# Optimization experiments

Measured on AMD Instinct MI355X. Metric: run time of the kernel, lower is better.

The kernel has to match this reference:

```python
import jax, jax.numpy as jnp
import numpy as np

NT, NC = 100000, 25000
ETT, ECT = 800000, 400000
DIN_T, DIN_C = 64, 32
H, C = 4, 32
HID = H * C  # 128
SLOPE = 0.2  # GATConv LeakyReLU negative slope


def setup_inputs() -> dict:
    key = jax.random.key(0)
    ks = jax.random.split(key, 24)
    def p(i, shape, s=0.05):
        return jax.random.normal(ks[i], shape, dtype=jnp.float32) * s
    return {
        'x_target': jax.random.normal(ks[0], (NT, DIN_T), dtype=jnp.float32),
        'x_context': jax.random.normal(ks[1], (NC, DIN_C), dtype=jnp.float32),
        'edge_tt': jax.random.randint(ks[2], (2, ETT), 0, NT),
        'edge_ct_src': jax.random.randint(ks[3], (ECT,), 0, NC),
        'edge_ct_dst': jax.random.randint(ks[4], (ECT,), 0, NT),
        'W_pre_t': p(5, (DIN_T, HID)), 'b_pre_t': jnp.zeros((HID,), jnp.float32),
        'W_pre_c': p(6, (DIN_C, HID)), 'b_pre_c': jnp.zeros((HID,), jnp.float32),
        'W_sd': p(7, (HID, HID)), 'att_src_sd': p(8, (H, C)), 'att_dst_sd': p(9, (H, C)), 'b_sd': jnp.zeros((HID,), jnp.float32),
        'W_ds': p(10, (HID, HID)), 'att_src_ds': p(11, (H, C)), 'att_dst_ds': p(12, (H, C)), 'b_ds': jnp.zeros((HID,), jnp.float32),
        'W_ct_src': p(13, (HID, HID)), 'W_ct_dst': p(14, (HID, HID)), 'att_src_ct': p(15, (H, C)), 'att_dst_ct': p(16, (H, C)), 'b_ct': jnp.zeros((HID,), jnp.float32),
        'W_out': p(17, (HID, HID)), 'b_out': jnp.zeros((HID,), jnp.float32),
    }


def _gat(h_src, h_dst, att_s, att_d, src, dst, n_dst, bias):
    # h_src: [N_src,H,C] transformed src feats; h_dst: [N_dst,H,C]
    a_s = jnp.einsum('nhc,hc->nh', h_src, att_s)  # [N_src,H]
    a_d = jnp.einsum('nhc,hc->nh', h_dst, att_d)  # [N_dst,H]
    e = a_s[src] + a_d[dst]                        # [E,H]
    e = jnp.where(e > 0, e, SLOPE * e)             # LeakyReLU(0.2)
    m = jax.ops.segment_max(e, dst, num_segments=n_dst)  # stable softmax per dst
    ex = jnp.exp(e - m[dst])
    den = jax.ops.segment_sum(ex, dst, num_segments=n_dst)
    alpha = ex / den[dst]                          # [E,H]
    msg = h_src[src] * alpha[:, :, None]           # [E,H,C]
    out = jax.ops.segment_sum(msg, dst, num_segments=n_dst)
    return out.reshape(n_dst, H * C) + bias


def reference(x_target, x_context, edge_tt, edge_ct_src, edge_ct_dst,
              W_pre_t, b_pre_t, W_pre_c, b_pre_c,
              W_sd, att_src_sd, att_dst_sd, b_sd,
              W_ds, att_src_ds, att_dst_ds, b_ds,
              W_ct_src, W_ct_dst, att_src_ct, att_dst_ct, b_ct,
              W_out, b_out):
    # HeteroDictLinear pretransform + relu
    h_t = jax.nn.relu(x_target @ W_pre_t + b_pre_t)   # [NT,128]
    h_c = jax.nn.relu(x_context @ W_pre_c + b_pre_c)  # [NC,128]
    res = h_t
    # DirGATConv on (target,to,target): forward + reversed, each w/ self-loops
    loops = jnp.arange(NT)
    src_f = jnp.concatenate([edge_tt[0], loops]); dst_f = jnp.concatenate([edge_tt[1], loops])
    src_r = jnp.concatenate([edge_tt[1], loops]); dst_r = jnp.concatenate([edge_tt[0], loops])
    hs = (h_t @ W_sd).reshape(NT, H, C)
    out_sd = _gat(hs, hs, att_src_sd, att_dst_sd, src_f, dst_f, NT, b_sd)
    hd = (h_t @ W_ds).reshape(NT, H, C)
    out_ds = _gat(hd, hd, att_src_ds, att_dst_ds, src_r, dst_r, NT, b_ds)
    out_tt = 0.5 * out_sd + 0.5 * out_ds  # (1-alpha), alpha with alpha=0.5
    # bipartite GATConv on (context,to,target), no self loops
    hcs = (h_c @ W_ct_src).reshape(NC, H, C)
    htd = (h_t @ W_ct_dst).reshape(NT, H, C)
    out_ct = _gat(hcs, htd, att_src_ct, att_dst_ct, edge_ct_src, edge_ct_dst, NT, b_ct)
    # HeteroConv aggr='mean' over the two edge types hitting 'target'
    x = 0.5 * (out_tt + out_ct)
    x = jax.nn.relu(x + res)  # skip connection + relu
    return x @ W_out + b_out
```

## Files before the change

kernel.cpp:

```cpp
#include <hip/hip_runtime.h>
#include <cstdint>
#include <cstddef>

typedef unsigned short u16;
typedef unsigned int u32;

#define NT 100000
#define NC 25000
#define ETT 800000
#define ECT 400000
#define SLOPE 0.2f
#define LOG2E 1.4426950408889634f
#define OFFS (NT + 4)

#define NBK 782
#define NBLK 256
#define CHT ((ETT + NBLK - 1) / NBLK)
#define CHC ((ECT + NBLK - 1) / NBLK)
#define TOTC (3 * NBK * NBLK)
#define NSB ((TOTC + 4095) / 4096)
#define FILL_CAP 4096

#define PT_BLK ((NT + 63) / 64)
#define CT_BLK ((NC + 63) / 64)

#define LROWS1 782
#define LROWS2 781
#define GOH 50048
#define G1BLK (GOH / 16)
#define G2BLK ((NT - GOH + 15) / 16)
#define OB1 (GOH / 64)
#define OB2 ((NT - GOH + 63) / 64)

typedef __attribute__((ext_vector_type(8))) short bf16x8;
typedef __attribute__((ext_vector_type(4))) float f32x4;

__device__ __forceinline__ u16 f2bf(float f) {
  u32 u = __float_as_uint(f);
  u32 r = (u >> 16) & 1u;
  return (u16)((u + 0x7fffu + r) >> 16);
}
__device__ __forceinline__ float lof(u32 p) { return __uint_as_float(p << 16); }
__device__ __forceinline__ float hif(u32 p) { return __uint_as_float(p & 0xffff0000u); }

__device__ __forceinline__ void compute_bpre(const int* __restrict__ bsum, int* s_bpre) {
  const int t = threadIdx.x;
  const int v = (t < NSB) ? bsum[t] : 0;
  s_bpre[t] = v;
  __syncthreads();
  for (int d = 1; d < 256; d <<= 1) {
    const int u = (t >= d) ? s_bpre[t - d] : 0;
    __syncthreads();
    s_bpre[t] += u;
    __syncthreads();
  }
  const int incl = s_bpre[t];
  __syncthreads();
  s_bpre[t] = incl - v;
  __syncthreads();
}

__global__ __launch_bounds__(256) void transform_hist_kernel(
    const int* __restrict__ tt_src, const int* __restrict__ tt_dst,
    const int* __restrict__ ect_d, int* __restrict__ cntblk,
    const float* __restrict__ Wsd, const float* __restrict__ AsSd, const float* __restrict__ AdSd,
    const float* __restrict__ Wds, const float* __restrict__ AsDs, const float* __restrict__ AdDs,
    const float* __restrict__ Wout,
    u16* __restrict__ bf_sd, u16* __restrict__ bf_ds, u16* __restrict__ bf_out,
    const float* __restrict__ Wcd, const float* __restrict__ attD,
    const float* __restrict__ bsd, const float* __restrict__ bds, const float* __restrict__ bct,
    float* __restrict__ cbias,
    const float* __restrict__ x_t, const float* __restrict__ Wpt, const float* __restrict__ bpt,
    u16* __restrict__ h_t, float* __restrict__ aD,
    const float* __restrict__ x_c, const float* __restrict__ Wpc, const float* __restrict__ bpc,
    const float* __restrict__ Wcs, const float* __restrict__ attS,
    u16* __restrict__ hc_bf, float* __restrict__ aS_c)
{
  __shared__ __align__(16) char smem[51200];
  const int t = threadIdx.x;

  if (blockIdx.x < NBLK) {
    int* h = (int*)smem;
    const int b = blockIdx.x;
    for (int i = t; i < 3 * NBK; i += 256) h[i] = 0;
    __syncthreads();
    const int lo = b * CHT, hi = min(lo + CHT, ETT);
    for (int i = lo + t; i < hi; i += 256) {
      atomicAdd(&h[tt_dst[i] >> 7], 1);
      atomicAdd(&h[NBK + (tt_src[i] >> 7)], 1);
    }
    const int lo2 = b * CHC, hi2 = min(lo2 + CHC, ECT);
    for (int i = lo2 + t; i < hi2; i += 256)
      atomicAdd(&h[2 * NBK + (ect_d[i] >> 7)], 1);
    __syncthreads();
    for (int i = t; i < 3 * NBK; i += 256)
      cntblk[(size_t)i * NBLK + b] = h[i];
    return;
  }

  const int b = blockIdx.x - NBLK;

  if (b < 4) {
    if (b == 3) {
      if (t < 128) cbias[t] = 0.25f * bsd[t] + 0.25f * bds[t] + 0.5f * bct[t];
      return;
    }
    float* fS = (float*)smem;
    float* fD = fS + 512;
    const float* W = (b == 0) ? Wsd : (b == 1) ? Wds : Wout;
    const float* As = (b == 0) ? AsSd : AsDs;
    const float* Ad = (b == 0) ? AdSd : AdDs;
    u16* out = (b == 0) ? bf_sd : (b == 1) ? bf_ds : bf_out;
    const int tiles = (b == 2) ? 8 : 9;
    if (b < 2) {
      if (t < 128) {
        for (int hh = 0; hh < 4; ++hh) {
          float s1 = 0.f, s2 = 0.f;
          for (int c = 0; c < 32; ++c) {
            const float wv = W[t * 128 + hh * 32 + c];
            s1 = fmaf(wv, As[hh * 32 + c], s1);
            s2 = fmaf(wv, Ad[hh * 32 + c], s2);
          }
          fS[t * 4 + hh] = s1 * LOG2E; fD[t * 4 + hh] = s2 * LOG2E;
        }
      }
      __syncthreads();
    }
    const int total = tiles * 4 * 64 * 8;
    for (int i = t; i < total; i += 256) {
      const int j = i & 7, lane = (i >> 3) & 63, ks = (i >> 9) & 3, ti = i >> 11;
      const int k = ks * 32 + (lane >> 4) * 8 + j;
      const int n = ti * 16 + (lane & 15);
      float v;
      if (n < 128) v = W[k * 128 + n];
      else if (n < 132) v = fS[k * 4 + (n - 128)];
      else if (n < 136) v = fD[k * 4 + (n - 132)];
      else v = 0.f;
      out[i] = f2bf(v);
    }
    return;
  }

  if (b < 4 + PT_BLK) {
    float (*s_xt)[68] = (float(*)[68])smem;
    float (*s_W)[128] = (float(*)[128])(smem + 17408);
    float* s_fold     = (float*)(smem + 17408 + 16384);
    const int row0 = (b - 4) * 64;
    for (int g = 0; g < 4; ++g) {
      const int lr = g * 16 + (t >> 4);
      const int k4 = (t & 15) * 4;
      const int grow = row0 + lr;
      float4 f = make_float4(0.f, 0.f, 0.f, 0.f);
      if (grow < NT) f = *(const float4*)(x_t + (size_t)grow * 64 + k4);
      s_xt[k4 + 0][lr] = f.x; s_xt[k4 + 1][lr] = f.y;
      s_xt[k4 + 2][lr] = f.z; s_xt[k4 + 3][lr] = f.w;
    }
    if (t < 128) {
      for (int hh = 0; hh < 4; ++hh) {
        float s = 0.f;
        for (int c = 0; c < 32; ++c)
          s = fmaf(Wcd[t * 128 + hh * 32 + c], attD[hh * 32 + c], s);
        s_fold[t * 4 + hh] = s * LOG2E;
      }
    }
    const int rg = t >> 4;
    const int cg = t & 15;
    float acc[4][8];
    for (int r = 0; r < 4; ++r)
      for (int j = 0; j < 8; ++j)
        acc[r][j] = bpt[cg * 4 + (j & 3) + (j >> 2) * 64];
    for (int kc = 0; kc < 64; kc += 32) {
      for (int j = 0; j < 4; ++j) {
        const int idx = t + j * 256;
        const int k = idx >> 5, c4 = (idx & 31) * 4;
        *(float4*)&s_W[k][c4] = *(const float4*)(Wpt + (size_t)(kc + k) * 128 + c4);
      }
      __syncthreads();
#pragma unroll 8
      for (int k = 0; k < 32; ++k) {
        const float4 xa = *(const float4*)&s_xt[kc + k][rg * 4];
        const float4 w0 = *(const float4*)&s_W[k][cg * 4];
        const float4 w1 = *(const float4*)&s_W[k][cg * 4 + 64];
        const float xr[4] = {xa.x, xa.y, xa.z, xa.w};
        for (int r = 0; r < 4; ++r) {
          acc[r][0] = fmaf(xr[r], w0.x, acc[r][0]);
          acc[r][1] = fmaf(xr[r], w0.y, acc[r][1]);
          acc[r][2] = fmaf(xr[r], w0.z, acc[r][2]);
          acc[r][3] = fmaf(xr[r], w0.w, acc[r][3]);
          acc[r][4] = fmaf(xr[r], w1.x, acc[r][4]);
          acc[r][5] = fmaf(xr[r], w1.y, acc[r][5]);
          acc[r][6] = fmaf(xr[r], w1.z, acc[r][6]);
          acc[r][7] = fmaf(xr[r], w1.w, acc[r][7]);
        }
      }
      __syncthreads();
    }
    for (int r = 0; r < 4; ++r) {
      const int grow = row0 + rg * 4 + r;
      float v[8];
      for (int j = 0; j < 8; ++j) v[j] = fmaxf(acc[r][j], 0.f);
      float p0 = 0.f, p1 = 0.f, p2 = 0.f, p3 = 0.f;
      for (int j = 0; j < 8; ++j) {
        const int col = cg * 4 + (j & 3) + ((j >> 2) * 64);
        const float4 f4 = *(const float4*)&s_fold[col * 4];
        p0 = fmaf(v[j], f4.x, p0); p1 = fmaf(v[j], f4.y, p1);
        p2 = fmaf(v[j], f4.z, p2); p3 = fmaf(v[j], f4.w, p3);
      }
      if (grow < NT) {
        uint2 pk;
        pk.x = (u32)f2bf(v[0]) | ((u32)f2bf(v[1]) << 16);
        pk.y = (u32)f2bf(v[2]) | ((u32)f2bf(v[3]) << 16);
        *(uint2*)(h_t + (size_t)grow * 128 + cg * 4) = pk;
        pk.x = (u32)f2bf(v[4]) | ((u32)f2bf(v[5]) << 16);
        pk.y = (u32)f2bf(v[6]) | ((u32)f2bf(v[7]) << 16);
        *(uint2*)(h_t + (size_t)grow * 128 + cg * 4 + 64) = pk;
      }
      for (int m = 1; m < 16; m <<= 1) {
        p0 += __shfl_xor(p0, m); p1 += __shfl_xor(p1, m);
        p2 += __shfl_xor(p2, m); p3 += __shfl_xor(p3, m);
      }
      if (cg == 0 && grow < NT)
        *(float4*)(aD + (size_t)grow * 4) = make_float4(p0, p1, p2, p3);
    }
    return;
  }

  {
    float (*s_ht)[68]  = (float(*)[68])smem;
    float (*s_W2)[128] = (float(*)[128])(smem + 34816);
    float (*s_xc)[68]  = (float(*)[68])smem;
    const int row0 = (b - 4 - PT_BLK) * 64;
    for (int g = 0; g < 2; ++g) {
      const int lr = g * 32 + (t >> 3);
      const int k4 = (t & 7) * 4;
      const int grow = row0 + lr;
      float4 f = make_float4(0.f, 0.f, 0.f, 0.f);
      if (grow < NC) f = *(const float4*)(x_c + (size_t)grow * 32 + k4);
      s_xc[k4 + 0][lr] = f.x; s_xc[k4 + 1][lr] = f.y;
      s_xc[k4 + 2][lr] = f.z; s_xc[k4 + 3][lr] = f.w;
    }
    for (int j = 0; j < 4; ++j) {
      const int idx = t + j * 256;
      const int k = idx >> 5, c4 = (idx & 31) * 4;
      *(float4*)&s_W2[k][c4] = *(const float4*)(Wpc + (size_t)k * 128 + c4);
    }
    __syncthreads();
    const int rg = t >> 4, cg = t & 15;
    float acc1[4][8];
    for (int r = 0; r < 4; ++r)
      for (int j = 0; j < 8; ++j)
        acc1[r][j] = bpc[cg * 4 + (j & 3) + (j >> 2) * 64];
#pragma unroll 8
    for (int k = 0; k < 32; ++k) {
      const float4 xa = *(const float4*)&s_xc[k][rg * 4];
      const float4 w0 = *(const float4*)&s_W2[k][cg * 4];
      const float4 w1 = *(const float4*)&s_W2[k][cg * 4 + 64];
      const float xr[4] = {xa.x, xa.y, xa.z, xa.w};
      for (int r = 0; r < 4; ++r) {
        acc1[r][0] = fmaf(xr[r], w0.x, acc1[r][0]);
        acc1[r][1] = fmaf(xr[r], w0.y, acc1[r][1]);
        acc1[r][2] = fmaf(xr[r], w0.z, acc1[r][2]);
        acc1[r][3] = fmaf(xr[r], w0.w, acc1[r][3]);
        acc1[r][4] = fmaf(xr[r], w1.x, acc1[r][4]);
        acc1[r][5] = fmaf(xr[r], w1.y, acc1[r][5]);
        acc1[r][6] = fmaf(xr[r], w1.z, acc1[r][6]);
        acc1[r][7] = fmaf(xr[r], w1.w, acc1[r][7]);
      }
    }
    __syncthreads();
    for (int r = 0; r < 4; ++r) {
      const int lr = rg * 4 + r;
      for (int j = 0; j < 8; ++j) {
        const int col = cg * 4 + (j & 3) + ((j >> 2) * 64);
        s_ht[col][lr] = fmaxf(acc1[r][j], 0.f);
      }
    }
    for (int j = 0; j < 4; ++j) {
      const int idx = t + j * 256;
      const int k = idx >> 5, c4 = (idx & 31) * 4;
      *(float4*)&s_W2[k][c4] = *(const float4*)(Wcs + (size_t)k * 128 + c4);
    }
    __syncthreads();
    float acc2[4][8];
    for (int r = 0; r < 4; ++r)
      for (int j = 0; j < 8; ++j) acc2[r][j] = 0.f;
    for (int kc = 0; kc < 128; kc += 32) {
#pragma unroll 8
      for (int k = 0; k < 32; ++k) {
        const float4 xa = *(const float4*)&s_ht[kc + k][rg * 4];
        const float4 w0 = *(const float4*)&s_W2[k][cg * 4];
        const float4 w1 = *(const float4*)&s_W2[k][cg * 4 + 64];
        const float xr[4] = {xa.x, xa.y, xa.z, xa.w};
        for (int r = 0; r < 4; ++r) {
          acc2[r][0] = fmaf(xr[r], w0.x, acc2[r][0]);
          acc2[r][1] = fmaf(xr[r], w0.y, acc2[r][1]);
          acc2[r][2] = fmaf(xr[r], w0.z, acc2[r][2]);
          acc2[r][3] = fmaf(xr[r], w0.w, acc2[r][3]);
          acc2[r][4] = fmaf(xr[r], w1.x, acc2[r][4]);
          acc2[r][5] = fmaf(xr[r], w1.y, acc2[r][5]);
          acc2[r][6] = fmaf(xr[r], w1.z, acc2[r][6]);
          acc2[r][7] = fmaf(xr[r], w1.w, acc2[r][7]);
        }
      }
      if (kc < 96) {
        __syncthreads();
        for (int j = 0; j < 4; ++j) {
          const int idx = t + j * 256;
          const int k = idx >> 5, c4 = (idx & 31) * 4;
          *(float4*)&s_W2[k][c4] = *(const float4*)(Wcs + (size_t)(kc + 32 + k) * 128 + c4);
        }
        __syncthreads();
      }
    }
    const int h2 = cg >> 3;
    const float4 at0 = *(const float4*)(attS + cg * 4);
    const float4 at1 = *(const float4*)(attS + cg * 4 + 64);
    for (int r = 0; r < 4; ++r) {
      const int grow = row0 + rg * 4 + r;
      float pa = acc2[r][0] * at0.x + acc2[r][1] * at0.y +
                 acc2[r][2] * at0.z + acc2[r][3] * at0.w;
      float pb = acc2[r][4] * at1.x + acc2[r][5] * at1.y +
                 acc2[r][6] * at1.z + acc2[r][7] * at1.w;
      if (grow < NC) {
        uint2 pk;
        pk.x = (u32)f2bf(acc2[r][0]) | ((u32)f2bf(acc2[r][1]) << 16);
        pk.y = (u32)f2bf(acc2[r][2]) | ((u32)f2bf(acc2[r][3]) << 16);
        *(uint2*)(hc_bf + (size_t)grow * 128 + cg * 4) = pk;
        pk.x = (u32)f2bf(acc2[r][4]) | ((u32)f2bf(acc2[r][5]) << 16);
        pk.y = (u32)f2bf(acc2[r][6]) | ((u32)f2bf(acc2[r][7]) << 16);
        *(uint2*)(hc_bf + (size_t)grow * 128 + cg * 4 + 64) = pk;
      }
      for (int m = 1; m < 8; m <<= 1) {
        pa += __shfl_xor(pa, m);
        pb += __shfl_xor(pb, m);
      }
      if ((cg & 7) == 0 && grow < NC) {
        aS_c[(size_t)grow * 4 + h2] = pa * LOG2E;
        aS_c[(size_t)grow * 4 + 2 + h2] = pb * LOG2E;
      }
    }
  }
}

__global__ __launch_bounds__(256) void scan2_blk_kernel(const int* __restrict__ in,
    int* __restrict__ out, int* __restrict__ bsum)
{
  const int t = threadIdx.x, b = blockIdx.x;
  const int idx = b * 4096 + t * 16;
  int v[16];
  int s = 0;
  if (idx < TOTC) {
#pragma unroll
    for (int q = 0; q < 4; ++q) {
      const int4 qq = *(const int4*)(in + idx + q * 4);
      v[q * 4 + 0] = s; s += qq.x;
      v[q * 4 + 1] = s; s += qq.y;
      v[q * 4 + 2] = s; s += qq.z;
      v[q * 4 + 3] = s; s += qq.w;
    }
  } else {
    for (int j = 0; j < 16; ++j) v[j] = 0;
  }
  __shared__ int sh[256];
  sh[t] = s;
  __syncthreads();
  for (int d = 1; d < 256; d <<= 1) {
    const int u = (t >= d) ? sh[t - d] : 0;
    __syncthreads();
    sh[t] += u;
    __syncthreads();
  }
  const int excl = (t == 0) ? 0 : sh[t - 1];
  if (idx < TOTC) {
#pragma unroll
    for (int q = 0; q < 4; ++q) {
      int4 qo;
      qo.x = excl + v[q * 4 + 0]; qo.y = excl + v[q * 4 + 1];
      qo.z = excl + v[q * 4 + 2]; qo.w = excl + v[q * 4 + 3];
      *(int4*)(out + idx + q * 4) = qo;
    }
  }
  if (t == 255) bsum[b] = sh[255];
}

__device__ __forceinline__ void logits2_body(float (*lds)[16][148], int blk, int rbase,
    const short* __restrict__ A, const short* __restrict__ Bsd, const short* __restrict__ Bds,
    u16* __restrict__ hs, float* __restrict__ aSsd, float* __restrict__ aDsd,
    u16* __restrict__ hd, float* __restrict__ aSds, float* __restrict__ aDds, int M)
{
  const int t = threadIdx.x;
  const int wv = t >> 6, lane = t & 63;
  const int quad = lane >> 4, l16 = lane & 15;
  const int row0 = rbase + blk * 64 + wv * 16;
  const int arow = min(row0 + l16, M - 1);
  const short* ap = A + (size_t)arow * 128 + quad * 8;
  bf16x8 af[4];
  for (int ks = 0; ks < 4; ++ks) af[ks] = *(const bf16x8*)(ap + ks * 32);
  const int row = row0 + l16;
  const int idx = lane & 7, rr = lane >> 3;
  for (int pass = 0; pass < 2; ++pass) {
    const short* B = pass ? Bds : Bsd;
    u16* outb = pass ? hd : hs;
    float* aS = pass ? aSds : aSsd;
    float* aD = pass ? aDds : aDsd;
    f32x4 acc[9];
    for (int ti = 0; ti < 9; ++ti) acc[ti] = (f32x4){0.f, 0.f, 0.f, 0.f};
    for (int ks = 0; ks < 4; ++ks)
      for (int ti = 0; ti < 9; ++ti) {
        const bf16x8 bf = *(const bf16x8*)(B + ((ti * 4 + ks) * 64 + lane) * 8);
        acc[ti] = __builtin_amdgcn_mfma_f32_16x16x32_bf16(af[ks], bf, acc[ti], 0, 0, 0);
      }
    for (int ti = 0; ti < 9; ++ti)
      for (int r = 0; r < 4; ++r)
        lds[wv][quad * 4 + r][ti * 16 + l16] = acc[ti][r];
    __syncthreads();
    if (row < M) {
      for (int g = 0; g < 8; ++g) {
        const f32x4 v = *(const f32x4*)&lds[wv][l16][g * 16 + quad * 4];
        uint2 pk;
        pk.x = (u32)f2bf(v[0]) | ((u32)f2bf(v[1]) << 16);
        pk.y = (u32)f2bf(v[2]) | ((u32)f2bf(v[3]) << 16);
        *(uint2*)(outb + (size_t)row * 128 + g * 16 + quad * 4) = pk;
      }
    }
    for (int p = 0; p < 2; ++p) {
      const int lr = p * 8 + rr;
      const int n = row0 + lr;
      if (n < M) {
        const float v = lds[wv][lr][128 + idx];
        if (idx < 4) aS[(size_t)n * 4 + idx] = v;
        else aD[(size_t)n * 4 + idx - 4] = v;
      }
    }
    __syncthreads();
  }
}

__global__ __launch_bounds__(256) void bin_logits2_kernel(
    const int* __restrict__ tt_src, const int* __restrict__ tt_dst,
    const int* __restrict__ ect_s, const int* __restrict__ ect_d,
    const int* __restrict__ scanned, const int* __restrict__ bsum, u32* __restrict__ bin,
    const short* __restrict__ A, const short* __restrict__ Bsd, const short* __restrict__ Bds,
    u16* __restrict__ hs, float* __restrict__ aSsd, float* __restrict__ aDsd,
    u16* __restrict__ hd, float* __restrict__ aSds, float* __restrict__ aDds, int M)
{
  __shared__ __align__(16) float ldsf[4][16][148];
  const int t = threadIdx.x;

  if (blockIdx.x < NBLK) {
    int* cur = (int*)&ldsf[0][0][0];
    int* s_bpre = cur + 3 * NBK;
    compute_bpre(bsum, s_bpre);
    const int b = blockIdx.x;
    for (int i = t; i < 3 * NBK; i += 256) {
      const int idx = i * NBLK + b;
      cur[i] = scanned[idx] + s_bpre[idx >> 12];
    }
    __syncthreads();
    const int lo = b * CHT, hi = min(lo + CHT, ETT);
    for (int i = lo + t; i < hi; i += 256) {
      const int s = tt_src[i], d = tt_dst[i];
      int p = atomicAdd(&cur[d >> 7], 1);
      bin[p] = ((u32)(d & 127) << 17) | (u32)s;
      p = atomicAdd(&cur[NBK + (s >> 7)], 1);
      bin[p] = ((u32)(s & 127) << 17) | (u32)d;
    }
    const int lo2 = b * CHC, hi2 = min(lo2 + CHC, ECT);
    for (int i = lo2 + t; i < hi2; i += 256) {
      const int s = ect_s[i], d = ect_d[i];
      const int p = atomicAdd(&cur[2 * NBK + (d >> 7)], 1);
      bin[p] = ((u32)(d & 127) << 17) | (u32)s;
    }
    return;
  }
  logits2_body(ldsf, blockIdx.x - NBLK, 0, A, Bsd, Bds,
               hs, aSsd, aDsd, hd, aSds, aDds, M);
}

__global__ __launch_bounds__(256) void fill_logits2_kernel(
    const int* __restrict__ scanned, const int* __restrict__ bsum, const u32* __restrict__ bin,
    int* __restrict__ offs, int* __restrict__ big_el,
    const short* __restrict__ A, const short* __restrict__ Bsd, const short* __restrict__ Bds,
    u16* __restrict__ hs, float* __restrict__ aSsd, float* __restrict__ aDsd,
    u16* __restrict__ hd, float* __restrict__ aSds, float* __restrict__ aDds, int M)
{
  __shared__ __align__(16) float ldsf[4][16][148];
  const int t = threadIdx.x;

  if (blockIdx.x < 3 * NBK) {
    int* base0 = (int*)&ldsf[0][0][0];
    int* s_cnt = base0;
    int* s_exc = base0 + 128;
    int* s_cur = base0 + 256;
    int* s_bpre = base0 + 384;
    int* s_el = base0 + 640;
    compute_bpre(bsum, s_bpre);
    const int rel = blockIdx.x / NBK;
    const int bucket = blockIdx.x - rel * NBK;
    if (t < 128) s_cnt[t] = 0;
    const int bi = blockIdx.x * NBLK;
    const int base = scanned[bi] + s_bpre[bi >> 12];
    const int nxt = (blockIdx.x == 3 * NBK - 1)
                        ? (2 * ETT + ECT)
                        : scanned[bi + NBLK] + s_bpre[(bi + NBLK) >> 12];
    __syncthreads();
    const int size = nxt - base;
    for (int i = t; i < size; i += 256)
      atomicAdd(&s_cnt[bin[base + i] >> 17], 1);
    __syncthreads();
    if (t < 128) s_exc[t] = s_cnt[t];
    __syncthreads();
    for (int d = 1; d < 128; d <<= 1) {
      int v = 0;
      if (t < 128 && t >= d) v = s_exc[t - d];
      __syncthreads();
      if (t < 128) s_exc[t] += v;
      __syncthreads();
    }
    const int relbase = rel * ETT;
    const int obase = base - relbase;
    int* off_rel = offs + (size_t)rel * OFFS;
    const int node0 = bucket * 128;
    if (t < 128) {
      const int excl = s_exc[t] - s_cnt[t];
      s_cur[t] = excl;
      if (node0 + t < NT) off_rel[node0 + t] = obase + excl;
    }
    if (t == 0 && bucket == NBK - 1) off_rel[NT] = obase + size;
    __syncthreads();
    int* el_rel = big_el + relbase;
    if (size <= FILL_CAP) {
      for (int i = t; i < size; i += 256) {
        const u32 e = bin[base + i];
        const int pos = atomicAdd(&s_cur[e >> 17], 1);
        s_el[pos] = (int)(e & 0x1FFFFu);
      }
      __syncthreads();
      for (int i = t; i < size; i += 256)
        el_rel[obase + i] = s_el[i];
    } else {
      for (int i = t; i < size; i += 256) {
        const u32 e = bin[base + i];
        const int pos = atomicAdd(&s_cur[e >> 17], 1);
        el_rel[obase + pos] = (int)(e & 0x1FFFFu);
      }
    }
    return;
  }
  logits2_body(ldsf, blockIdx.x - 3 * NBK, GOH, A, Bsd, Bds,
               hs, aSsd, aDsd, hd, aSds, aDds, M);
}

__device__ __forceinline__ void mfma_out_body(float (*lds)[16][132], int row0,
    const short* __restrict__ A, const short* __restrict__ B,
    const float* __restrict__ bias, float* __restrict__ out, int M)
{
  const int t = threadIdx.x;
  const int wv = t >> 6, lane = t & 63;
  const int quad = lane >> 4, l16 = lane & 15;
  const int r0 = row0 + wv * 16;
  const int arow = min(r0 + l16, M - 1);
  const short* ap = A + (size_t)arow * 128 + quad * 8;
  bf16x8 af[4];
  for (int ks = 0; ks < 4; ++ks) af[ks] = *(const bf16x8*)(ap + ks * 32);
  f32x4 acc[8];
  for (int ti = 0; ti < 8; ++ti) acc[ti] = (f32x4){0.f, 0.f, 0.f, 0.f};
  for (int ks = 0; ks < 4; ++ks)
    for (int ti = 0; ti < 8; ++ti) {
      const bf16x8 bf = *(const bf16x8*)(B + ((ti * 4 + ks) * 64 + lane) * 8);
      acc[ti] = __builtin_amdgcn_mfma_f32_16x16x32_bf16(af[ks], bf, acc[ti], 0, 0, 0);
    }
  for (int ti = 0; ti < 8; ++ti)
    for (int r = 0; r < 4; ++r)
      lds[wv][quad * 4 + r][ti * 16 + l16] = acc[ti][r];
  __syncthreads();
  const int row = r0 + l16;
  if (row < M) {
    for (int g = 0; g < 8; ++g) {
      const int col = g * 16 + quad * 4;
      f32x4 v = *(const f32x4*)&lds[wv][l16][col];
      const f32x4 b4 = *(const f32x4*)(bias + col);
      v = v + b4;
      *(f32x4*)(out + (size_t)row * 128 + col) = v;
    }
  }
}

__global__ __launch_bounds__(256) void mfma_out_kernel(
    const short* __restrict__ A, const short* __restrict__ B,
    const float* __restrict__ bias, float* __restrict__ out, int rbase, int M)
{
  __shared__ __align__(16) float lds[4][16][132];
  mfma_out_body(lds, rbase + blockIdx.x * 64, A, B, bias, out, M);
}

__device__ __forceinline__ void gat_pipe16(const int* __restrict__ off,
    const int* __restrict__ el, const float* __restrict__ aS, const float* __restrict__ aD,
    const u16* __restrict__ hb, int d, int h, int cb, int self_loop, float w,
    float* __restrict__ acc)
{
  const float ad = aD[(size_t)d * 4 + h];
  const int beg = off[d];
  const int m = off[d + 1] - beg;
  const int cnt = m + self_loop;
  if (cnt <= 0) return;
  float den = 0.f;
  float a0 = 0.f, a1 = 0.f, a2 = 0.f, a3 = 0.f, a4 = 0.f, a5 = 0.f, a6 = 0.f, a7 = 0.f;
  int sB = (1 < m) ? el[beg + 1] : d;
  {
    const int sA0 = (0 < m) ? el[beg] : d;
    float eA = aS[(size_t)sA0 * 4 + h];
    uint4 pA = *(const uint4*)(hb + (size_t)sA0 * 128 + cb);
    for (int k = 0; k < cnt; ++k) {
      const int sC = (k + 2 < m) ? el[beg + k + 2] : d;
      const float eB = aS[(size_t)sB * 4 + h];
      const uint4 pB = *(const uint4*)(hb + (size_t)sB * 128 + cb);
      float ea = eA + ad;
      ea = ea > 0.f ? ea : SLOPE * ea;
      const float ex = exp2f(ea);
      den += ex;
      a0 = fmaf(ex, lof(pA.x), a0); a1 = fmaf(ex, hif(pA.x), a1);
      a2 = fmaf(ex, lof(pA.y), a2); a3 = fmaf(ex, hif(pA.y), a3);
      a4 = fmaf(ex, lof(pA.z), a4); a5 = fmaf(ex, hif(pA.z), a5);
      a6 = fmaf(ex, lof(pA.w), a6); a7 = fmaf(ex, hif(pA.w), a7);
      eA = eB; pA = pB; sB = sC;
    }
  }
  const float s = w / den;
  acc[0] = fmaf(a0, s, acc[0]); acc[1] = fmaf(a1, s, acc[1]);
  acc[2] = fmaf(a2, s, acc[2]); acc[3] = fmaf(a3, s, acc[3]);
  acc[4] = fmaf(a4, s, acc[4]); acc[5] = fmaf(a5, s, acc[5]);
  acc[6] = fmaf(a6, s, acc[6]); acc[7] = fmaf(a7, s, acc[7]);
}

__device__ __forceinline__ void gather_body(int d,
    const int* __restrict__ off_f, const int* __restrict__ el_f,
    const float* __restrict__ aS_sd, const float* __restrict__ aD_sd, const u16* __restrict__ hs,
    const int* __restrict__ off_r, const int* __restrict__ el_r,
    const float* __restrict__ aS_ds, const float* __restrict__ aD_ds, const u16* __restrict__ hd,
    const int* __restrict__ off_c, const int* __restrict__ el_c,
    const float* __restrict__ aS_ct, const float* __restrict__ aD_ct, const u16* __restrict__ hc,
    const u16* __restrict__ skip, const float* __restrict__ cbias, u16* __restrict__ x)
{
  const int lg = threadIdx.x & 15;
  const int h = lg >> 2;
  const int cb = lg * 8;
  float acc[8];
  for (int i = 0; i < 8; ++i) acc[i] = 0.f;
  gat_pipe16(off_f, el_f, aS_sd, aD_sd, hs, d, h, cb, 1, 0.25f, acc);
  gat_pipe16(off_r, el_r, aS_ds, aD_ds, hd, d, h, cb, 1, 0.25f, acc);
  gat_pipe16(off_c, el_c, aS_ct, aD_ct, hc, d, h, cb, 0, 0.5f, acc);
  const uint4 sk = *(const uint4*)(skip + (size_t)d * 128 + cb);
  const float4 cb0 = *(const float4*)(cbias + cb);
  const float4 cb1 = *(const float4*)(cbias + cb + 4);
  const float o0 = fmaxf(acc[0] + cb0.x + lof(sk.x), 0.f);
  const float o1 = fmaxf(acc[1] + cb0.y + hif(sk.x), 0.f);
  const float o2 = fmaxf(acc[2] + cb0.z + lof(sk.y), 0.f);
  const float o3 = fmaxf(acc[3] + cb0.w + hif(sk.y), 0.f);
  const float o4 = fmaxf(acc[4] + cb1.x + lof(sk.z), 0.f);
  const float o5 = fmaxf(acc[5] + cb1.y + hif(sk.z), 0.f);
  const float o6 = fmaxf(acc[6] + cb1.z + lof(sk.w), 0.f);
  const float o7 = fmaxf(acc[7] + cb1.w + hif(sk.w), 0.f);
  uint4 r;
  r.x = (u32)f2bf(o0) | ((u32)f2bf(o1) << 16);
  r.y = (u32)f2bf(o2) | ((u32)f2bf(o3) << 16);
  r.z = (u32)f2bf(o4) | ((u32)f2bf(o5) << 16);
  r.w = (u32)f2bf(o6) | ((u32)f2bf(o7) << 16);
  *(uint4*)(x + (size_t)d * 128 + cb) = r;
}

__global__ __launch_bounds__(256) void gather_all_kernel(
    const int* __restrict__ off_f, const int* __restrict__ el_f,
    const float* __restrict__ aS_sd, const float* __restrict__ aD_sd, const u16* __restrict__ hs,
    const int* __restrict__ off_r, const int* __restrict__ el_r,
    const float* __restrict__ aS_ds, const float* __restrict__ aD_ds, const u16* __restrict__ hd,
    const int* __restrict__ off_c, const int* __restrict__ el_c,
    const float* __restrict__ aS_ct, const float* __restrict__ aD_ct, const u16* __restrict__ hc,
    const u16* __restrict__ skip, const float* __restrict__ cbias, u16* __restrict__ x)
{
  const int d = blockIdx.x * 16 + (threadIdx.x >> 4);
  if (d >= NT) return;
  gather_body(d, off_f, el_f, aS_sd, aD_sd, hs, off_r, el_r, aS_ds, aD_ds, hd,
              off_c, el_c, aS_ct, aD_ct, hc, skip, cbias, x);
}

__global__ __launch_bounds__(256) void gather_out_kernel(
    const int* __restrict__ off_f, const int* __restrict__ el_f,
    const float* __restrict__ aS_sd, const float* __restrict__ aD_sd, const u16* __restrict__ hs,
    const int* __restrict__ off_r, const int* __restrict__ el_r,
    const float* __restrict__ aS_ds, const float* __restrict__ aD_ds, const u16* __restrict__ hd,
    const int* __restrict__ off_c, const int* __restrict__ el_c,
    const float* __restrict__ aS_ct, const float* __restrict__ aD_ct, const u16* __restrict__ hc,
    const u16* __restrict__ skip, const float* __restrict__ cbias, u16* __restrict__ x,
    const short* __restrict__ B, const float* __restrict__ bias, float* __restrict__ out, int M)
{
  __shared__ __align__(16) float lds[4][16][132];
  if (blockIdx.x < G2BLK) {
    const int d = GOH + blockIdx.x * 16 + (threadIdx.x >> 4);
    if (d >= NT) return;
    gather_body(d, off_f, el_f, aS_sd, aD_sd, hs, off_r, el_r, aS_ds, aD_ds, hd,
                off_c, el_c, aS_ct, aD_ct, hc, skip, cbias, x);
    return;
  }
  mfma_out_body(lds, (blockIdx.x - G2BLK) * 64, (const short*)x, B, bias, out, M);
}

extern "C" void kernel_launch(void* const* d_in, const int* in_sizes, int n_in,
                              void* d_out, int out_size, void* d_ws, size_t ws_size,
                              hipStream_t stream)
{
  const float* x_t   = (const float*)d_in[0];
  const float* x_c   = (const float*)d_in[1];
  const int*   e_tt  = (const int*)d_in[2];
  const int*   ect_s = (const int*)d_in[3];
  const int*   ect_d = (const int*)d_in[4];
  const float* Wpt = (const float*)d_in[5];   const float* bpt = (const float*)d_in[6];
  const float* Wpc = (const float*)d_in[7];   const float* bpc = (const float*)d_in[8];
  const float* Wsd = (const float*)d_in[9];   const float* As_sd = (const float*)d_in[10];
  const float* Ad_sd = (const float*)d_in[11]; const float* bsd = (const float*)d_in[12];
  const float* Wds = (const float*)d_in[13];  const float* As_ds = (const float*)d_in[14];
  const float* Ad_ds = (const float*)d_in[15]; const float* bds = (const float*)d_in[16];
  const float* Wcs = (const float*)d_in[17];  const float* Wcd = (const float*)d_in[18];
  const float* As_ct = (const float*)d_in[19]; const float* Ad_ct = (const float*)d_in[20];
  const float* bct = (const float*)d_in[21];
  const float* Wout = (const float*)d_in[22]; const float* bout = (const float*)d_in[23];

  char* p = (char*)d_ws;
  size_t off = 0;
  auto alloc = [&](size_t bytes) { char* r = p + off; off += (bytes + 255) & ~(size_t)255; return r; };
  u16* ht_bf   = (u16*)alloc((size_t)NT * 128 * 2);
  u16* hs_bf   = (u16*)alloc((size_t)NT * 128 * 2);
  u16* hd_bf   = (u16*)alloc((size_t)NT * 128 * 2);
  u16* hc_bf   = (u16*)alloc((size_t)NC * 128 * 2);
  u16* x_bf    = (u16*)alloc((size_t)NT * 128 * 2);
  float* aS_sd = (float*)alloc((size_t)NT * 4 * 4);
  float* aD_sd = (float*)alloc((size_t)NT * 4 * 4);
  float* aS_ds = (float*)alloc((size_t)NT * 4 * 4);
  float* aD_ds = (float*)alloc((size_t)NT * 4 * 4);
  float* aS_ct = (float*)alloc((size_t)NC * 4 * 4);
  float* aD_ct = (float*)alloc((size_t)NT * 4 * 4);
  int* cntblk  = (int*)alloc((size_t)TOTC * 4);
  int* scanned = (int*)alloc((size_t)TOTC * 4);
  u32* bin     = (u32*)alloc((size_t)(2 * ETT + ECT) * 4);
  int* big_el  = (int*)alloc((size_t)(2 * ETT + ECT) * 4);
  int* offs    = (int*)alloc((size_t)3 * OFFS * 4);
  int* bsum    = (int*)alloc((size_t)NSB * 4);
  float* cbias   = (float*)alloc(128 * 4);
  u16* bfrag_sd  = (u16*)alloc((size_t)9 * 4 * 64 * 8 * 2);
  u16* bfrag_ds  = (u16*)alloc((size_t)9 * 4 * 64 * 8 * 2);
  u16* bfrag_out = (u16*)alloc((size_t)8 * 4 * 64 * 8 * 2);

  int* off_f = offs;
  int* off_r = offs + OFFS;
  int* off_c = offs + 2 * OFFS;
  int* el_f = big_el;
  int* el_r = big_el + ETT;
  int* el_c = big_el + 2 * ETT;

  const int* tt_src = e_tt;
  const int* tt_dst = e_tt + ETT;

  transform_hist_kernel<<<NBLK + 4 + PT_BLK + CT_BLK, 256, 0, stream>>>(
      tt_src, tt_dst, ect_d, cntblk,
      Wsd, As_sd, Ad_sd, Wds, As_ds, Ad_ds, Wout,
      bfrag_sd, bfrag_ds, bfrag_out,
      Wcd, Ad_ct, bsd, bds, bct, cbias,
      x_t, Wpt, bpt, ht_bf, aD_ct,
      x_c, Wpc, bpc, Wcs, As_ct, hc_bf, aS_ct);

  scan2_blk_kernel<<<NSB, 256, 0, stream>>>(cntblk, scanned, bsum);

  bin_logits2_kernel<<<NBLK + LROWS1, 256, 0, stream>>>(
      tt_src, tt_dst, ect_s, ect_d, scanned, bsum, bin,
      (const short*)ht_bf, (const short*)bfrag_sd, (const short*)bfrag_ds,
      hs_bf, aS_sd, aD_sd, hd_bf, aS_ds, aD_ds, NT);

  fill_logits2_kernel<<<3 * NBK + LROWS2, 256, 0, stream>>>(
      scanned, bsum, bin, offs, big_el,
      (const short*)ht_bf, (const short*)bfrag_sd, (const short*)bfrag_ds,
      hs_bf, aS_sd, aD_sd, hd_bf, aS_ds, aD_ds, NT);

  gather_all_kernel<<<G1BLK, 256, 0, stream>>>(
      off_f, el_f, aS_sd, aD_sd, hs_bf,
      off_r, el_r, aS_ds, aD_ds, hd_bf,
      off_c, el_c, aS_ct, aD_ct, hc_bf,
      ht_bf, cbias, x_bf);

  gather_out_kernel<<<G2BLK + OB1, 256, 0, stream>>>(
      off_f, el_f, aS_sd, aD_sd, hs_bf,
      off_r, el_r, aS_ds, aD_ds, hd_bf,
      off_c, el_c, aS_ct, aD_ct, hc_bf,
      ht_bf, cbias, x_bf,
      (const short*)bfrag_out, bout, (float*)d_out, NT);

  mfma_out_kernel<<<OB2, 256, 0, stream>>>((const short*)x_bf, (const short*)bfrag_out,
                                           bout, (float*)d_out, GOH, NT);
}
```

Before: 409.7 us.

## Move all logits GEMM into bin kernel, slim fill kernel, direct-store output GEMM

```diff
diff --git a/kernel.cpp b/kernel.cpp
--- a/kernel.cpp
+++ b/kernel.cpp
@@ -23,12 +23,11 @@
 
 #define PT_BLK ((NT + 63) / 64)
 #define CT_BLK ((NC + 63) / 64)
-
-#define LROWS1 782
-#define LROWS2 781
+#define GM_BLK ((NT + 63) / 64)
+
 #define GOH 50048
 #define G1BLK (GOH / 16)
-#define G2BLK ((NT - GOH + 15) / 16)
+#define G2BLK ((NT - GOH) / 16)
 #define OB1 (GOH / 64)
 #define OB2 ((NT - GOH + 63) / 64)
 
@@ -383,7 +382,7 @@
   if (t == 255) bsum[b] = sh[255];
 }
 
-__device__ __forceinline__ void logits2_body(float (*lds)[16][148], int blk, int rbase,
+__device__ __forceinline__ void logits2_body(float (*lds)[16][148], int blk,
     const short* __restrict__ A, const short* __restrict__ Bsd, const short* __restrict__ Bds,
     u16* __restrict__ hs, float* __restrict__ aSsd, float* __restrict__ aDsd,
     u16* __restrict__ hd, float* __restrict__ aSds, float* __restrict__ aDds, int M)
@@ -391,7 +390,7 @@
   const int t = threadIdx.x;
   const int wv = t >> 6, lane = t & 63;
   const int quad = lane >> 4, l16 = lane & 15;
-  const int row0 = rbase + blk * 64 + wv * 16;
+  const int row0 = blk * 64 + wv * 16;
   const int arow = min(row0 + l16, M - 1);
   const short* ap = A + (size_t)arow * 128 + quad * 8;
   bf16x8 af[4];
@@ -473,85 +472,71 @@
     }
     return;
   }
-  logits2_body(ldsf, blockIdx.x - NBLK, 0, A, Bsd, Bds,
+  logits2_body(ldsf, blockIdx.x - NBLK, A, Bsd, Bds,
                hs, aSsd, aDsd, hd, aSds, aDds, M);
 }
 
-__global__ __launch_bounds__(256) void fill_logits2_kernel(
-    const int* __restrict__ scanned, const int* __restrict__ bsum, const u32* __restrict__ bin,
-    int* __restrict__ offs, int* __restrict__ big_el,
-    const short* __restrict__ A, const short* __restrict__ Bsd, const short* __restrict__ Bds,
-    u16* __restrict__ hs, float* __restrict__ aSsd, float* __restrict__ aDsd,
-    u16* __restrict__ hd, float* __restrict__ aSds, float* __restrict__ aDds, int M)
-{
-  __shared__ __align__(16) float ldsf[4][16][148];
+__global__ __launch_bounds__(256) void bucket_fill_kernel(const int* __restrict__ scanned,
+    const int* __restrict__ bsum, const u32* __restrict__ bin,
+    int* __restrict__ offs, int* __restrict__ big_el)
+{
+  __shared__ int s_cnt[128], s_exc[128], s_cur[128], s_bpre[256];
+  __shared__ int s_el[FILL_CAP];
   const int t = threadIdx.x;
-
-  if (blockIdx.x < 3 * NBK) {
-    int* base0 = (int*)&ldsf[0][0][0];
-    int* s_cnt = base0;
-    int* s_exc = base0 + 128;
-    int* s_cur = base0 + 256;
-    int* s_bpre = base0 + 384;
-    int* s_el = base0 + 640;
-    compute_bpre(bsum, s_bpre);
-    const int rel = blockIdx.x / NBK;
-    const int bucket = blockIdx.x - rel * NBK;
-    if (t < 128) s_cnt[t] = 0;
-    const int bi = blockIdx.x * NBLK;
-    const int base = scanned[bi] + s_bpre[bi >> 12];
-    const int nxt = (blockIdx.x == 3 * NBK - 1)
-                        ? (2 * ETT + ECT)
-                        : scanned[bi + NBLK] + s_bpre[(bi + NBLK) >> 12];
-    __syncthreads();
-    const int size = nxt - base;
+  compute_bpre(bsum, s_bpre);
+  const int rel = blockIdx.x / NBK;
+  const int bucket = blockIdx.x - rel * NBK;
+  if (t < 128) s_cnt[t] = 0;
+  const int bi = blockIdx.x * NBLK;
+  const int base = scanned[bi] + s_bpre[bi >> 12];
+  const int nxt = (blockIdx.x == 3 * NBK - 1)
+                      ? (2 * ETT + ECT)
+                      : scanned[bi + NBLK] + s_bpre[(bi + NBLK) >> 12];
+  __syncthreads();
+  const int size = nxt - base;
+  for (int i = t; i < size; i += 256)
+    atomicAdd(&s_cnt[bin[base + i] >> 17], 1);
+  __syncthreads();
+  if (t < 128) s_exc[t] = s_cnt[t];
+  __syncthreads();
+  for (int d = 1; d < 128; d <<= 1) {
+    int v = 0;
+    if (t < 128 && t >= d) v = s_exc[t - d];
+    __syncthreads();
+    if (t < 128) s_exc[t] += v;
+    __syncthreads();
+  }
+  const int relbase = rel * ETT;
+  const int obase = base - relbase;
+  int* off_rel = offs + (size_t)rel * OFFS;
+  const int node0 = bucket * 128;
+  if (t < 128) {
+    const int excl = s_exc[t] - s_cnt[t];
+    s_cur[t] = excl;
+    if (node0 + t < NT) off_rel[node0 + t] = obase + excl;
+  }
+  if (t == 0 && bucket == NBK - 1) off_rel[NT] = obase + size;
+  __syncthreads();
+  int* el_rel = big_el + relbase;
+  if (size <= FILL_CAP) {
+    for (int i = t; i < size; i += 256) {
+      const u32 e = bin[base + i];
+      const int pos = atomicAdd(&s_cur[e >> 17], 1);
+      s_el[pos] = (int)(e & 0x1FFFFu);
+    }
+    __syncthreads();
     for (int i = t; i < size; i += 256)
-      atomicAdd(&s_cnt[bin[base + i] >> 17], 1);
-    __syncthreads();
-    if (t < 128) s_exc[t] = s_cnt[t];
-    __syncthreads();
-    for (int d = 1; d < 128; d <<= 1) {
-      int v = 0;
-      if (t < 128 && t >= d) v = s_exc[t - d];
-      __syncthreads();
-      if (t < 128) s_exc[t] += v;
-      __syncthreads();
-    }
-    const int relbase = rel * ETT;
-    const int obase = base - relbase;
-    int* off_rel = offs + (size_t)rel * OFFS;
-    const int node0 = bucket * 128;
-    if (t < 128) {
-      const int excl = s_exc[t] - s_cnt[t];
-      s_cur[t] = excl;
-      if (node0 + t < NT) off_rel[node0 + t] = obase + excl;
-    }
-    if (t == 0 && bucket == NBK - 1) off_rel[NT] = obase + size;
-    __syncthreads();
-    int* el_rel = big_el + relbase;
-    if (size <= FILL_CAP) {
-      for (int i = t; i < size; i += 256) {
-        const u32 e = bin[base + i];
-        const int pos = atomicAdd(&s_cur[e >> 17], 1);
-        s_el[pos] = (int)(e & 0x1FFFFu);
-      }
-      __syncthreads();
-      for (int i = t; i < size; i += 256)
-        el_rel[obase + i] = s_el[i];
-    } else {
-      for (int i = t; i < size; i += 256) {
-        const u32 e = bin[base + i];
-        const int pos = atomicAdd(&s_cur[e >> 17], 1);
-        el_rel[obase + pos] = (int)(e & 0x1FFFFu);
-      }
-    }
-    return;
-  }
-  logits2_body(ldsf, blockIdx.x - 3 * NBK, GOH, A, Bsd, Bds,
-               hs, aSsd, aDsd, hd, aSds, aDds, M);
-}
-
-__device__ __forceinline__ void mfma_out_body(float (*lds)[16][132], int row0,
+      el_rel[obase + i] = s_el[i];
+  } else {
+    for (int i = t; i < size; i += 256) {
+      const u32 e = bin[base + i];
+      const int pos = atomicAdd(&s_cur[e >> 17], 1);
+      el_rel[obase + pos] = (int)(e & 0x1FFFFu);
+    }
+  }
+}
+
+__device__ __forceinline__ void mfma_out_direct(int row0,
     const short* __restrict__ A, const short* __restrict__ B,
     const float* __restrict__ bias, float* __restrict__ out, int M)
 {
@@ -570,18 +555,17 @@
       const bf16x8 bf = *(const bf16x8*)(B + ((ti * 4 + ks) * 64 + lane) * 8);
       acc[ti] = __builtin_amdgcn_mfma_f32_16x16x32_bf16(af[ks], bf, acc[ti], 0, 0, 0);
     }
-  for (int ti = 0; ti < 8; ++ti)
-    for (int r = 0; r < 4; ++r)
-      lds[wv][quad * 4 + r][ti * 16 + l16] = acc[ti][r];
-  __syncthreads();
-  const int row = r0 + l16;
-  if (row < M) {
-    for (int g = 0; g < 8; ++g) {
-      const int col = g * 16 + quad * 4;
-      f32x4 v = *(const f32x4*)&lds[wv][l16][col];
-      const f32x4 b4 = *(const f32x4*)(bias + col);
-      v = v + b4;
-      *(f32x4*)(out + (size_t)row * 128 + col) = v;
+  float bcol[8];
+#pragma unroll
+  for (int ti = 0; ti < 8; ++ti) bcol[ti] = bias[ti * 16 + l16];
+#pragma unroll
+  for (int r = 0; r < 4; ++r) {
+    const int row = r0 + quad * 4 + r;
+    if (row < M) {
+      float* orow = out + (size_t)row * 128 + l16;
+#pragma unroll
+      for (int ti = 0; ti < 8; ++ti)
+        orow[ti * 16] = acc[ti][r] + bcol[ti];
     }
   }
 }
@@ -590,8 +574,7 @@
     const short* __restrict__ A, const short* __restrict__ B,
     const float* __restrict__ bias, float* __restrict__ out, int rbase, int M)
 {
-  __shared__ __align__(16) float lds[4][16][132];
-  mfma_out_body(lds, rbase + blockIdx.x * 64, A, B, bias, out, M);
+  mfma_out_direct(rbase + blockIdx.x * 64, A, B, bias, out, M);
 }
 
 __device__ __forceinline__ void gat_pipe16(const int* __restrict__ off,
@@ -694,7 +677,6 @@
     const u16* __restrict__ skip, const float* __restrict__ cbias, u16* __restrict__ x,
     const short* __restrict__ B, const float* __restrict__ bias, float* __restrict__ out, int M)
 {
-  __shared__ __align__(16) float lds[4][16][132];
   if (blockIdx.x < G2BLK) {
     const int d = GOH + blockIdx.x * 16 + (threadIdx.x >> 4);
     if (d >= NT) return;
@@ -702,7 +684,7 @@
                 off_c, el_c, aS_ct, aD_ct, hc, skip, cbias, x);
     return;
   }
-  mfma_out_body(lds, (blockIdx.x - G2BLK) * 64, (const short*)x, B, bias, out, M);
+  mfma_out_direct((blockIdx.x - G2BLK) * 64, (const short*)x, B, bias, out, M);
 }
 
 extern "C" void kernel_launch(void* const* d_in, const int* in_sizes, int n_in,
@@ -770,15 +752,12 @@
 
   scan2_blk_kernel<<<NSB, 256, 0, stream>>>(cntblk, scanned, bsum);
 
-  bin_logits2_kernel<<<NBLK + LROWS1, 256, 0, stream>>>(
+  bin_logits2_kernel<<<NBLK + GM_BLK, 256, 0, stream>>>(
       tt_src, tt_dst, ect_s, ect_d, scanned, bsum, bin,
       (const short*)ht_bf, (const short*)bfrag_sd, (const short*)bfrag_ds,
       hs_bf, aS_sd, aD_sd, hd_bf, aS_ds, aD_ds, NT);
 
-  fill_logits2_kernel<<<3 * NBK + LROWS2, 256, 0, stream>>>(
-      scanned, bsum, bin, offs, big_el,
-      (const short*)ht_bf, (const short*)bfrag_sd, (const short*)bfrag_ds,
-      hs_bf, aS_sd, aD_sd, hd_bf, aS_ds, aD_ds, NT);
+  bucket_fill_kernel<<<3 * NBK, 256, 0, stream>>>(scanned, bsum, bin, offs, big_el);
 
   gather_all_kernel<<<G1BLK, 256, 0, stream>>>(
       off_f, el_f, aS_sd, aD_sd, hs_bf,
```

After: 389.2 us. 5.0% less time.
